# Performance work log

Measured on AMD Instinct MI355X. Metric: run time of the kernel, lower is better.

The kernel has to match this reference:

```python
import jax, jax.numpy as jnp
import numpy as np

N, E, B, H, L = 50000, 500000, 64, 64, 4


def setup_inputs() -> dict:
    key = jax.random.key(0)
    ks = jax.random.split(key, 32)
    def w(k, shp, fan_in):
        s = 1.0 / np.sqrt(fan_in)
        return jax.random.uniform(k, shp, jnp.float32, -s, s)
    inp = {
        "v0": jax.random.normal(ks[0], (N, 1), jnp.float32),
        "v1": jax.random.normal(ks[1], (N, 1), jnp.float32),
        "dist": jax.random.uniform(ks[2], (E, 1), jnp.float32),
        "edge_index": jax.random.randint(ks[3], (2, E), 0, N, jnp.int32),
        "batch": jnp.sort(jax.random.randint(ks[4], (N,), 0, B, jnp.int32)),
        "batch_size": B,
        # embeddings / per-input linears
        "wte": jax.random.normal(ks[5], (2, H), jnp.float32),
        "W_in0": w(ks[6], (H, 1), 1), "b_in0": w(ks[7], (H,), 1),
        "W_in1": w(ks[8], (H, 1), 1), "b_in1": w(ks[9], (H,), 1),
        "W_out0": w(ks[10], (1, H), H), "b_out0": w(ks[11], (1,), H),
        "W_out1": w(ks[12], (1, H), H), "b_out1": w(ks[13], (1,), H),
        "W_edge": w(ks[14], (H, 1), 1), "b_edge": w(ks[15], (H,), 1),
        # shared GraphBlock (ModuleList([block]*L) shares weights)
        "W_el": w(ks[16], (H, 2 * H), 2 * H), "b_el": w(ks[17], (H,), 2 * H),
        "W_n1": w(ks[18], (4 * H, 3 * H), 3 * H), "b_n1": w(ks[19], (4 * H,), 3 * H),
        "W_n2": w(ks[20], (H, 4 * H), 4 * H), "b_n2": w(ks[21], (H,), 4 * H),
        "W_gl": w(ks[22], (H, 2 * H), 2 * H), "b_gl": w(ks[23], (H,), 2 * H),
        # shared LSTMCell
        "W_ih": w(ks[24], (4 * H, H), H), "W_hh": w(ks[25], (4 * H, H), H),
        "b_ih": w(ks[26], (4 * H,), H), "b_hh": w(ks[27], (4 * H,), H),
    }
    return inp


def _forward(v0, v1, dist, edge_index, batch, batch_size,
             wte, W_in0, b_in0, W_in1, b_in1, W_out0, b_out0, W_out1, b_out1,
             W_edge, b_edge, W_el, b_el, W_n1, b_n1, W_n2, b_n2, W_gl, b_gl,
             W_ih, W_hh, b_ih, b_hh):
    # x = sum_i (type_embedding_i + Linear_i(v_i))  -> [N, H]
    x = (wte[0] + v0 @ W_in0.T + b_in0) + (wte[1] + v1 @ W_in1.T + b_in1)
    e = dist @ W_edge.T + b_edge                      # [E, H]
    u = jnp.zeros((batch_size, x.shape[-1]), x.dtype)  # [B, H]
    row, col = edge_index[0], edge_index[1]
    n_nodes = x.shape[0]
    cs = []
    for _ in range(L):  # shared weights across layers (faithful to [block]*L)
        # edge MLP on gathered source features, scatter-max to destination nodes
        msg = jax.nn.relu(jnp.concatenate([x[row], e], axis=-1) @ W_el.T + b_el)
        agg = jax.ops.segment_max(msg, col, num_segments=n_nodes)
        agg = jnp.where(jnp.isfinite(agg), agg, 0.0)  # empty segments -> 0
        # node MLP with residual
        h1 = jax.nn.relu(jnp.concatenate([agg, x, u[batch]], axis=-1) @ W_n1.T + b_n1)
        x = x + h1 @ W_n2.T + b_n2
        # global update: per-graph max over nodes
        x_u = jax.ops.segment_max(x, batch, num_segments=batch_size)
        x_u = jnp.where(jnp.isfinite(x_u), x_u, 0.0)
        u = u + jax.nn.relu(jnp.concatenate([x_u, u], axis=-1) @ W_gl.T + b_gl)
        # LSTMCell with zero initial (h, c) every layer (hidden_states=None path)
        gates = u @ W_ih.T + b_ih + b_hh  # h_prev = 0 so W_hh term vanishes
        i_g, f_g, g_g, o_g = jnp.split(gates, 4, axis=-1)
        c = jax.nn.sigmoid(i_g) * jnp.tanh(g_g)        # c_prev = 0
        u = jax.nn.sigmoid(o_g) * jnp.tanh(c)
        cs.append(c)
    outs = jnp.stack([x @ W_out0.T + b_out0, x @ W_out1.T + b_out1])  # [2, N, 1]
    return outs, jnp.stack(cs)  # ([2,N,1], [L,B,H])


def reference(v0, v1, dist, edge_index, batch, batch_size,
              wte, W_in0, b_in0, W_in1, b_in1, W_out0, b_out0, W_out1, b_out1,
              W_edge, b_edge, W_el, b_el, W_n1, b_n1, W_n2, b_n2, W_gl, b_gl,
              W_ih, W_hh, b_ih, b_hh):
    return _forward(v0, v1, dist, edge_index, batch, batch_size,
                    wte, W_in0, b_in0, W_in1, b_in1, W_out0, b_out0, W_out1, b_out1,
                    W_edge, b_edge, W_el, b_el, W_n1, b_n1, W_n2, b_n2, W_gl, b_gl,
                    W_ih, W_hh, b_ih, b_hh)
```

## Files before the change

kernel.cpp:

```cpp
#include <hip/hip_runtime.h>


typedef __attribute__((ext_vector_type(8))) short short8;
typedef __attribute__((ext_vector_type(4))) float f32x4;

__device__ __forceinline__ unsigned short f2bf(float f) {
  union { float f; unsigned u; } v; v.f = f;
  unsigned r = v.u + 0x7FFFu + ((v.u >> 16) & 1u);
  return (unsigned short)(r >> 16);
}
__device__ __forceinline__ float bf2f(unsigned short s) {
  return __uint_as_float((unsigned)s << 16);
}
__device__ __forceinline__ unsigned enc_ordered(float f) {
  unsigned u = __float_as_uint(f);
  return (u >> 31) ? ~u : (u | 0x80000000u);
}

__global__ void k_prep_pq(const float* __restrict__ W_el, const float* __restrict__ b_el,
                          const float* __restrict__ W_edge, const float* __restrict__ b_edge,
                          const float* __restrict__ wte,
                          const float* __restrict__ Wi0, const float* __restrict__ bi0,
                          const float* __restrict__ Wi1, const float* __restrict__ bi1,
                          float* __restrict__ p, float* __restrict__ q,
                          float* __restrict__ c0, float* __restrict__ c1,
                          float* __restrict__ c2) {
  int h = threadIdx.x;
  float pp = 0.f, qq = 0.f, s0 = 0.f, s1 = 0.f, s2 = 0.f;
  for (int k = 0; k < 64; ++k) {
    float w2 = W_el[h * 128 + 64 + k];
    pp += w2 * W_edge[k];
    qq += w2 * b_edge[k];
    float w1 = W_el[h * 128 + k];
    float base = wte[k] + wte[64 + k] + bi0[k] + bi1[k];
    s0 += w1 * base;
    s1 += w1 * Wi0[k];
    s2 += w1 * Wi1[k];
  }
  p[h] = pp; q[h] = qq + b_el[h];
  c0[h] = s0; c1[h] = s1; c2[h] = s2;
}

__global__ void k_init(const float* __restrict__ v0, const float* __restrict__ v1,
                       const float* __restrict__ wte,
                       const float* __restrict__ Wi0, const float* __restrict__ bi0,
                       const float* __restrict__ Wi1, const float* __restrict__ bi1,
                       const int* __restrict__ batch,
                       int* __restrict__ gstart, int* __restrict__ gend,
                       float* __restrict__ x,
                       float* __restrict__ u, unsigned* __restrict__ xu_enc,
                       unsigned short* __restrict__ W1b, unsigned short* __restrict__ W2b,
                       unsigned short* __restrict__ Welb,
                       const float* __restrict__ W_n1, const float* __restrict__ W_n2,
                       const float* __restrict__ W_el,
                       int* __restrict__ deg, int* __restrict__ cur, int N) {
  int gt = blockIdx.x * 256 + threadIdx.x;
  int NH = N * 64;
  if (gt < NH) {
    int n = gt >> 6, h = gt & 63;
    x[gt] = wte[h] + wte[64 + h] + bi0[h] + bi1[h] + v0[n] * Wi0[h] + v1[n] * Wi1[h];
    if (h == 0) {
      int bg = batch[n];
      if (n == 0 || batch[n - 1] != bg) gstart[bg] = n;
      if (n == N - 1 || batch[n + 1] != bg) gend[bg] = n + 1;
    }
    return;
  }
  int i = gt - NH;
  if (i < 4096) {
    u[i] = 0.f;
  } else if (i < 8192) {
    xu_enc[i - 4096] = 0x007FFFFFu;
  } else if (i < 8192 + 49152) {
    int j = i - 8192;
    W1b[j] = f2bf(W_n1[j]);
  } else if (i < 8192 + 49152 + 16384) {
    int j = i - 57344;
    W2b[j] = f2bf(W_n2[j]);
  } else if (i < 77824) {
    int j = i - 73728;
    Welb[j] = f2bf(W_el[(j >> 6) * 128 + (j & 63)]);
  } else if (i < 77824 + N) {
    deg[i - 77824] = 0;
  } else if (i < 77824 + 2 * N) {
    cur[i - 77824 - N] = 0;
  }
}

__global__ __launch_bounds__(256) void k_hist(const int* __restrict__ eidx,
                                              int* __restrict__ deg, int E) {
  int e = blockIdx.x * 256 + threadIdx.x;
  if (e < E) atomicAdd(&deg[eidx[E + e]], 1);
}

__global__ __launch_bounds__(256) void k_scan1(const int* __restrict__ deg,
                                               int* __restrict__ off,
                                               int* __restrict__ bsum, int N) {
  __shared__ int s[256];
  int b = blockIdx.x, t = threadIdx.x;
  int i0 = b * 512 + t * 2;
  int v0 = (i0 < N) ? deg[i0] : 0;
  int v1 = (i0 + 1 < N) ? deg[i0 + 1] : 0;
  int sum = v0 + v1;
  s[t] = sum;
  __syncthreads();
  for (int d = 1; d < 256; d <<= 1) {
    int val = (t >= d) ? s[t - d] : 0;
    __syncthreads();
    s[t] += val;
    __syncthreads();
  }
  int excl = s[t] - sum;
  if (i0 < N) off[i0] = excl + v0;
  if (i0 + 1 < N) off[i0 + 1] = excl + v0 + v1;
  if (t == 255) bsum[b] = s[t];
}

__global__ void k_scan2(int* __restrict__ bsum, int nb) {
  __shared__ int s[128];
  int t = threadIdx.x;
  int v = (t < nb) ? bsum[t] : 0;
  s[t] = v;
  __syncthreads();
  for (int d = 1; d < 128; d <<= 1) {
    int val = (t >= d) ? s[t - d] : 0;
    __syncthreads();
    s[t] += val;
    __syncthreads();
  }
  if (t < nb) bsum[t] = s[t] - v;
}

__global__ __launch_bounds__(256) void k_scatter(const int* __restrict__ eidx,
                                                 const float* __restrict__ dist,
                                                 const int* __restrict__ off,
                                                 const int* __restrict__ bsum,
                                                 int* __restrict__ cur,
                                                 uint2* __restrict__ spack, int E) {
  int e = blockIdx.x * 256 + threadIdx.x;
  if (e >= E) return;
  int c = eidx[E + e];
  int base = (c == 0) ? 0 : (off[c - 1] + bsum[(c - 1) >> 9]);
  int pos = base + atomicAdd(&cur[c], 1);
  spack[pos] = make_uint2((unsigned)eidx[e] | ((unsigned)(c & 31) << 27),
                          __float_as_uint(dist[e]));
}

#define PROC(cc, gg)                                                     \
  do {                                                                   \
    int _c = (int)(cc);                                                  \
    if (_c != ccur) {                                                    \
      if (ccur >= 0) atomicMax(&aggi[ccur * 64 + lane], __float_as_int(m)); \
      ccur = _c; m = (gg);                                               \
    } else m = fmaxf(m, (gg));                                           \
  } while (0)

template <int MODE>
__global__ __launch_bounds__(256) void k_node(
    const int* __restrict__ off, const int* __restrict__ bsum,
    const uint2* __restrict__ spack,
    const float* __restrict__ p, const float* __restrict__ q,
    const float* __restrict__ c0, const float* __restrict__ c1,
    const float* __restrict__ c2,
    const float* __restrict__ v0, const float* __restrict__ v1,
    float* __restrict__ x, unsigned short* __restrict__ y_bf,
    const int* __restrict__ batch, const float* __restrict__ u,
    const unsigned short* __restrict__ W1b, const unsigned short* __restrict__ W2b,
    const unsigned short* __restrict__ Welb,
    const float* __restrict__ b_n1, const float* __restrict__ b_n2,
    unsigned* __restrict__ xu_enc,
    float* __restrict__ bmaxA, float* __restrict__ bmaxB,
    int* __restrict__ bgidA, int* __restrict__ bgidB,
    const float* __restrict__ Wo0, const float* __restrict__ bo0,
    const float* __restrict__ Wo1, const float* __restrict__ bo1,
    float* __restrict__ outp, int N) {
  __shared__ __align__(16) char inb[32 * 384];
  __shared__ __align__(16) char h1T[32 * 512];
  __shared__ uint2 smeta[256];
  __shared__ int sgb[32];
  int t = threadIdx.x;
  int n0 = blockIdx.x * 32;
  int lane = t & 63, wv = t >> 6;
  int lr = lane & 15;
  int lk8 = (lane >> 4) << 3;
  int jo = (lane >> 4) << 2;
  int swzr = (lr & 7) << 4;
  int h0 = wv * 16 + jo;

  float4 xo[2];
#pragma unroll
  for (int nt = 0; nt < 2; ++nt) {
    int node = n0 + nt * 16 + lr;
    xo[nt] = (node < N) ? *(const float4*)(x + (size_t)node * 64 + h0)
                        : make_float4(0.f, 0.f, 0.f, 0.f);
  }
  int nd_s = t >> 3, ko = t & 7;
  int node_s = n0 + nd_s;
  float4 ua = make_float4(0.f, 0.f, 0.f, 0.f), ub = ua;
  if (node_s < N) {
    int g = batch[node_s];
    const float4* u4 = (const float4*)u;
    ua = u4[g * 16 + ko * 2];
    ub = u4[g * 16 + ko * 2 + 1];
  }
  if (t < 32) sgb[t] = batch[min(n0 + t, N - 1)];
  float pv = p[lane], qv = q[lane];
  float c0v = 0.f, c1v = 0.f, c2v = 0.f;
  if (MODE == 0) { c0v = c0[lane]; c1v = c1[lane]; c2v = c2[lane]; }

  int* aggi = (int*)h1T;
#pragma unroll
  for (int i = 0; i < 8; ++i) aggi[t + i * 256] = 0;

#pragma unroll
  for (int nt = 0; nt < 2; ++nt) {
    int nd = nt * 16 + lr;
    unsigned lo = (unsigned)f2bf(xo[nt].x) | ((unsigned)f2bf(xo[nt].y) << 16);
    unsigned hi = (unsigned)f2bf(xo[nt].z) | ((unsigned)f2bf(xo[nt].w) << 16);
    *(uint2*)(inb + nd * 384 + ((128 + h0 * 2) ^ ((nd & 7) << 4))) = make_uint2(lo, hi);
  }
  {
    int swz = (nd_s & 7) << 4;
    uint4 uv;
    uv.x = f2bf(ua.x) | ((unsigned)f2bf(ua.y) << 16);
    uv.y = f2bf(ua.z) | ((unsigned)f2bf(ua.w) << 16);
    uv.z = f2bf(ub.x) | ((unsigned)f2bf(ub.y) << 16);
    uv.w = f2bf(ub.z) | ((unsigned)f2bf(ub.w) << 16);
    *(uint4*)(inb + nd_s * 384 + ((256 + ko * 16) ^ swz)) = uv;
  }
  __syncthreads();

  {
    int last = min(n0 + 31, N - 1);
    int ebase = (n0 == 0) ? 0 : (off[n0 - 1] + bsum[(n0 - 1) >> 9]);
    int eend = off[last] + bsum[last >> 9];
    int total = eend - ebase;
    int q4 = total >> 2;
    int wb = ebase + wv * q4;
    int we = (wv == 3) ? eend : (wb + q4);
    uint2* sm = smeta + wv * 64;
    const unsigned short* ybl = y_bf + lane;
    float m = 0.f;
    int ccur = -1;
    uint2 r = make_uint2(0u, 0u);
    if (wb < we) {
      int cnt = min(64, we - wb);
      if (lane < cnt) r = spack[wb + lane];
    }
    for (int cb = wb; cb < we; cb += 64) {
      int ccnt = min(64, we - cb);
      sm[lane] = r;
      int nb = cb + 64;
      if (nb < we) {
        int ncnt = we - nb;
        if (lane < ncnt) r = spack[nb + lane];
      }
      int i = 0;
      for (; i + 8 <= ccnt; i += 8) {
        uint2 e0 = sm[i], e1 = sm[i + 1], e2 = sm[i + 2], e3 = sm[i + 3];
        uint2 e4 = sm[i + 4], e5 = sm[i + 5], e6 = sm[i + 6], e7 = sm[i + 7];
        float y0, y1, y2, y3, y4, y5, y6, y7;
        if (MODE == 0) {
          int r0 = e0.x & 0x07FFFFFFu, r1 = e1.x & 0x07FFFFFFu;
          int r2 = e2.x & 0x07FFFFFFu, r3 = e3.x & 0x07FFFFFFu;
          int r4 = e4.x & 0x07FFFFFFu, r5 = e5.x & 0x07FFFFFFu;
          int r6 = e6.x & 0x07FFFFFFu, r7 = e7.x & 0x07FFFFFFu;
          y0 = fmaf(v1[r0], c2v, fmaf(v0[r0], c1v, c0v));
          y1 = fmaf(v1[r1], c2v, fmaf(v0[r1], c1v, c0v));
          y2 = fmaf(v1[r2], c2v, fmaf(v0[r2], c1v, c0v));
          y3 = fmaf(v1[r3], c2v, fmaf(v0[r3], c1v, c0v));
          y4 = fmaf(v1[r4], c2v, fmaf(v0[r4], c1v, c0v));
          y5 = fmaf(v1[r5], c2v, fmaf(v0[r5], c1v, c0v));
          y6 = fmaf(v1[r6], c2v, fmaf(v0[r6], c1v, c0v));
          y7 = fmaf(v1[r7], c2v, fmaf(v0[r7], c1v, c0v));
        } else {
          y0 = bf2f(ybl[(int)((e0.x & 0x07FFFFFFu) << 6)]);
          y1 = bf2f(ybl[(int)((e1.x & 0x07FFFFFFu) << 6)]);
          y2 = bf2f(ybl[(int)((e2.x & 0x07FFFFFFu) << 6)]);
          y3 = bf2f(ybl[(int)((e3.x & 0x07FFFFFFu) << 6)]);
          y4 = bf2f(ybl[(int)((e4.x & 0x07FFFFFFu) << 6)]);
          y5 = bf2f(ybl[(int)((e5.x & 0x07FFFFFFu) << 6)]);
          y6 = bf2f(ybl[(int)((e6.x & 0x07FFFFFFu) << 6)]);
          y7 = bf2f(ybl[(int)((e7.x & 0x07FFFFFFu) << 6)]);
        }
        float g0 = fmaxf(fmaf(__uint_as_float(e0.y), pv, y0 + qv), 0.f);
        float g1 = fmaxf(fmaf(__uint_as_float(e1.y), pv, y1 + qv), 0.f);
        float g2 = fmaxf(fmaf(__uint_as_float(e2.y), pv, y2 + qv), 0.f);
        float g3 = fmaxf(fmaf(__uint_as_float(e3.y), pv, y3 + qv), 0.f);
        float g4 = fmaxf(fmaf(__uint_as_float(e4.y), pv, y4 + qv), 0.f);
        float g5 = fmaxf(fmaf(__uint_as_float(e5.y), pv, y5 + qv), 0.f);
        float g6 = fmaxf(fmaf(__uint_as_float(e6.y), pv, y6 + qv), 0.f);
        float g7 = fmaxf(fmaf(__uint_as_float(e7.y), pv, y7 + qv), 0.f);
        PROC(e0.x >> 27, g0); PROC(e1.x >> 27, g1);
        PROC(e2.x >> 27, g2); PROC(e3.x >> 27, g3);
        PROC(e4.x >> 27, g4); PROC(e5.x >> 27, g5);
        PROC(e6.x >> 27, g6); PROC(e7.x >> 27, g7);
      }
      for (; i < ccnt; ++i) {
        uint2 e0 = sm[i];
        float y0;
        if (MODE == 0) {
          int r0 = e0.x & 0x07FFFFFFu;
          y0 = fmaf(v1[r0], c2v, fmaf(v0[r0], c1v, c0v));
        } else {
          y0 = bf2f(ybl[(int)((e0.x & 0x07FFFFFFu) << 6)]);
        }
        float g0 = fmaxf(fmaf(__uint_as_float(e0.y), pv, y0 + qv), 0.f);
        PROC(e0.x >> 27, g0);
      }
    }
    if (ccur >= 0) atomicMax(&aggi[ccur * 64 + lane], __float_as_int(m));
  }
  __syncthreads();

  {
    int swz = (nd_s & 7) << 4;
    const float4* ag4 = (const float4*)(h1T);
    float4 aa = ag4[nd_s * 16 + ko * 2];
    float4 ab = ag4[nd_s * 16 + ko * 2 + 1];
    uint4 av;
    av.x = f2bf(aa.x) | ((unsigned)f2bf(aa.y) << 16);
    av.y = f2bf(aa.z) | ((unsigned)f2bf(aa.w) << 16);
    av.z = f2bf(ab.x) | ((unsigned)f2bf(ab.y) << 16);
    av.w = f2bf(ab.z) | ((unsigned)f2bf(ab.w) << 16);
    *(uint4*)(inb + nd_s * 384 + ((ko * 16) ^ swz)) = av;
  }
  __syncthreads();

  int w = wv;

  f32x4 acc[4][2];
#pragma unroll
  for (int ot = 0; ot < 4; ++ot)
#pragma unroll
    for (int nt = 0; nt < 2; ++nt) acc[ot][nt] = (f32x4){0.f, 0.f, 0.f, 0.f};
  const unsigned short* W1p = W1b + (w * 64 + lr) * 192 + lk8;
#pragma unroll
  for (int ks = 0; ks < 6; ++ks) {
    int kb = ks * 64 + lk8 * 2;
    short8 b0 = *(const short8*)(inb + lr * 384 + (kb ^ swzr));
    short8 b1 = *(const short8*)(inb + (16 + lr) * 384 + (kb ^ swzr));
#pragma unroll
    for (int ot = 0; ot < 4; ++ot) {
      short8 a = *(const short8*)(W1p + ot * (16 * 192) + ks * 32);
      acc[ot][0] = __builtin_amdgcn_mfma_f32_16x16x32_bf16(a, b0, acc[ot][0], 0, 0, 0);
      acc[ot][1] = __builtin_amdgcn_mfma_f32_16x16x32_bf16(a, b1, acc[ot][1], 0, 0, 0);
    }
  }
  __syncthreads();
#pragma unroll
  for (int ot = 0; ot < 4; ++ot) {
    int o = w * 64 + ot * 16 + jo;
    float4 bs = *(const float4*)(b_n1 + o);
#pragma unroll
    for (int nt = 0; nt < 2; ++nt) {
      int nd = nt * 16 + lr;
      unsigned lo = (unsigned)f2bf(fmaxf(acc[ot][nt][0] + bs.x, 0.f)) |
                    ((unsigned)f2bf(fmaxf(acc[ot][nt][1] + bs.y, 0.f)) << 16);
      unsigned hi = (unsigned)f2bf(fmaxf(acc[ot][nt][2] + bs.z, 0.f)) |
                    ((unsigned)f2bf(fmaxf(acc[ot][nt][3] + bs.w, 0.f)) << 16);
      *(uint2*)(h1T + nd * 512 + ((o * 2) ^ ((nd & 7) << 4))) = make_uint2(lo, hi);
    }
  }
  __syncthreads();

  f32x4 acc2[2] = {{0.f, 0.f, 0.f, 0.f}, {0.f, 0.f, 0.f, 0.f}};
  const unsigned short* W2p = W2b + (w * 16 + lr) * 256 + lk8;
#pragma unroll
  for (int ks = 0; ks < 8; ++ks) {
    short8 a = *(const short8*)(W2p + ks * 32);
    int kb = ks * 64 + lk8 * 2;
    short8 b0 = *(const short8*)(h1T + lr * 512 + (kb ^ swzr));
    short8 b1 = *(const short8*)(h1T + (16 + lr) * 512 + (kb ^ swzr));
    acc2[0] = __builtin_amdgcn_mfma_f32_16x16x32_bf16(a, b0, acc2[0], 0, 0, 0);
    acc2[1] = __builtin_amdgcn_mfma_f32_16x16x32_bf16(a, b1, acc2[1], 0, 0, 0);
  }
  float4 b2 = *(const float4*)(b_n2 + h0);
  char* xnb = inb;
  float4 xn[2];
#pragma unroll
  for (int nt = 0; nt < 2; ++nt) {
    int nd = nt * 16 + lr;
    int node = n0 + nd;
    xn[nt].x = xo[nt].x + acc2[nt][0] + b2.x;
    xn[nt].y = xo[nt].y + acc2[nt][1] + b2.y;
    xn[nt].z = xo[nt].z + acc2[nt][2] + b2.z;
    xn[nt].w = xo[nt].w + acc2[nt][3] + b2.w;
    if (node >= N) xn[nt] = make_float4(0.f, 0.f, 0.f, 0.f);
    if (MODE != 2 && node < N) *(float4*)(x + (size_t)node * 64 + h0) = xn[nt];
    if (MODE != 2) {
      unsigned lo = (unsigned)f2bf(xn[nt].x) | ((unsigned)f2bf(xn[nt].y) << 16);
      unsigned hi = (unsigned)f2bf(xn[nt].z) | ((unsigned)f2bf(xn[nt].w) << 16);
      *(uint2*)(xnb + nd * 128 + ((h0 * 2) ^ ((nd & 7) << 4))) = make_uint2(lo, hi);
    }
  }

  {
    const float NEG = -__builtin_huge_valf();
    int gA = sgb[0], gB = sgb[31];
    float a0 = NEG, a1 = NEG, a2 = NEG, a3 = NEG;
    float e0 = NEG, e1 = NEG, e2 = NEG, e3 = NEG;
#pragma unroll
    for (int nt = 0; nt < 2; ++nt) {
      int nd = nt * 16 + lr;
      if (n0 + nd < N) {
        int g = sgb[nd];
        if (g == gA) {
          a0 = fmaxf(a0, xn[nt].x); a1 = fmaxf(a1, xn[nt].y);
          a2 = fmaxf(a2, xn[nt].z); a3 = fmaxf(a3, xn[nt].w);
        } else if (g == gB) {
          e0 = fmaxf(e0, xn[nt].x); e1 = fmaxf(e1, xn[nt].y);
          e2 = fmaxf(e2, xn[nt].z); e3 = fmaxf(e3, xn[nt].w);
        } else {
          unsigned* xe = xu_enc + g * 64 + h0;
          atomicMax(xe + 0, enc_ordered(xn[nt].x));
          atomicMax(xe + 1, enc_ordered(xn[nt].y));
          atomicMax(xe + 2, enc_ordered(xn[nt].z));
          atomicMax(xe + 3, enc_ordered(xn[nt].w));
        }
      }
    }
#pragma unroll
    for (int msk = 1; msk <= 8; msk <<= 1) {
      a0 = fmaxf(a0, __shfl_xor(a0, msk)); a1 = fmaxf(a1, __shfl_xor(a1, msk));
      a2 = fmaxf(a2, __shfl_xor(a2, msk)); a3 = fmaxf(a3, __shfl_xor(a3, msk));
      e0 = fmaxf(e0, __shfl_xor(e0, msk)); e1 = fmaxf(e1, __shfl_xor(e1, msk));
      e2 = fmaxf(e2, __shfl_xor(e2, msk)); e3 = fmaxf(e3, __shfl_xor(e3, msk));
    }
    if (lr == 0) {
      size_t base = (size_t)blockIdx.x * 64 + h0;
      bmaxA[base + 0] = a0; bmaxA[base + 1] = a1;
      bmaxA[base + 2] = a2; bmaxA[base + 3] = a3;
      bmaxB[base + 0] = e0; bmaxB[base + 1] = e1;
      bmaxB[base + 2] = e2; bmaxB[base + 3] = e3;
    }
    if (t == 0) {
      bgidA[blockIdx.x] = gA;
      bgidB[blockIdx.x] = (gB == gA) ? -1 : gB;
    }
  }
  __syncthreads();

  if (MODE != 2) {
    f32x4 acc3[2] = {{0.f, 0.f, 0.f, 0.f}, {0.f, 0.f, 0.f, 0.f}};
    const unsigned short* W3p = Welb + (w * 16 + lr) * 64 + lk8;
#pragma unroll
    for (int ks = 0; ks < 2; ++ks) {
      short8 a = *(const short8*)(W3p + ks * 32);
      int kb = ks * 64 + lk8 * 2;
      short8 b0 = *(const short8*)(xnb + lr * 128 + (kb ^ swzr));
      short8 b1 = *(const short8*)(xnb + (16 + lr) * 128 + (kb ^ swzr));
      acc3[0] = __builtin_amdgcn_mfma_f32_16x16x32_bf16(a, b0, acc3[0], 0, 0, 0);
      acc3[1] = __builtin_amdgcn_mfma_f32_16x16x32_bf16(a, b1, acc3[1], 0, 0, 0);
    }
    int o0 = w * 16 + jo;
#pragma unroll
    for (int nt = 0; nt < 2; ++nt) {
      int node = n0 + nt * 16 + lr;
      if (node < N) {
        unsigned lo = (unsigned)f2bf(acc3[nt][0]) | ((unsigned)f2bf(acc3[nt][1]) << 16);
        unsigned hi = (unsigned)f2bf(acc3[nt][2]) | ((unsigned)f2bf(acc3[nt][3]) << 16);
        *(uint2*)(y_bf + (size_t)node * 64 + o0) = make_uint2(lo, hi);
      }
    }
  } else {
    float4 w0 = *(const float4*)(Wo0 + h0);
    float4 w1 = *(const float4*)(Wo1 + h0);
    float* ow = (float*)h1T;
#pragma unroll
    for (int nt = 0; nt < 2; ++nt) {
      float p0 = xn[nt].x * w0.x + xn[nt].y * w0.y + xn[nt].z * w0.z + xn[nt].w * w0.w;
      float p1 = xn[nt].x * w1.x + xn[nt].y * w1.y + xn[nt].z * w1.z + xn[nt].w * w1.w;
      p0 += __shfl_xor(p0, 16); p0 += __shfl_xor(p0, 32);
      p1 += __shfl_xor(p1, 16); p1 += __shfl_xor(p1, 32);
      if (lane < 16) {
        ow[w * 64 + 0 + nt * 16 + lr] = p0;
        ow[w * 64 + 32 + nt * 16 + lr] = p1;
      }
    }
    __syncthreads();
    if (t < 64) {
      int oi = t >> 5, nd = t & 31;
      int node = n0 + nd;
      if (node < N) {
        float v = ow[0 * 64 + oi * 32 + nd] + ow[1 * 64 + oi * 32 + nd] +
                  ow[2 * 64 + oi * 32 + nd] + ow[3 * 64 + oi * 32 + nd];
        v += (oi ? bo1[0] : bo0[0]);
        outp[(size_t)oi * N + node] = v;
      }
    }
  }
}

__global__ __launch_bounds__(256) void k_graph(const int* __restrict__ gstart,
                                               const int* __restrict__ gend,
                                               const float* __restrict__ bmaxA,
                                               const float* __restrict__ bmaxB,
                                               const int* __restrict__ bgidA,
                                               const int* __restrict__ bgidB,
                                               unsigned* __restrict__ xu_enc,
                                               float* __restrict__ u,
                                               const float* __restrict__ W_gl,
                                               const float* __restrict__ b_gl,
                                               const float* __restrict__ W_ih,
                                               const float* __restrict__ b_ih,
                                               const float* __restrict__ b_hh,
                                               float* __restrict__ c_out) {
  __shared__ float red[4][3][64];
  __shared__ float xu_s[64], us[64], un[64];
  int g = blockIdx.x;
  int t = threadIdx.x, h = t & 63, qd = t >> 6;
  const float NEG = -__builtin_huge_valf();

  float m = NEG;
  int gs = gstart[g], ge = gend[g];
  if (gs < ge) {
    int bs = gs >> 5, be = (ge - 1) >> 5;
    for (int b = bs + qd; b <= be; b += 4) {
      if (bgidA[b] == g) m = fmaxf(m, bmaxA[(size_t)b * 64 + h]);
      if (bgidB[b] == g) m = fmaxf(m, bmaxB[(size_t)b * 64 + h]);
    }
  }
  red[qd][0][h] = m;
  __syncthreads();
  if (qd == 0) {
    m = fmaxf(fmaxf(red[0][0][h], red[1][0][h]), fmaxf(red[2][0][h], red[3][0][h]));
    unsigned Ev = xu_enc[g * 64 + h];
    float fd = (Ev & 0x80000000u) ? __uint_as_float(Ev & 0x7FFFFFFFu)
                                  : __uint_as_float(~Ev);
    m = fmaxf(m, fd);
    xu_enc[g * 64 + h] = 0x007FFFFFu;
    xu_s[h] = isfinite(m) ? m : 0.f;
    us[h] = u[g * 64 + h];
  }
  __syncthreads();

  float pre = 0.f;
  {
    const float* Wrow = W_gl + h * 128 + qd * 32;
    const float* src = (qd < 2) ? (xu_s + qd * 32) : (us + (qd - 2) * 32);
#pragma unroll 8
    for (int k = 0; k < 32; ++k) pre += src[k] * Wrow[k];
  }
  red[qd][0][h] = pre;
  __syncthreads();
  if (qd == 0) {
    float prs = red[0][0][h] + red[1][0][h] + red[2][0][h] + red[3][0][h] + b_gl[h];
    un[h] = us[h] + fmaxf(prs, 0.f);
  }
  __syncthreads();

  float gi = 0.f, gg = 0.f, go = 0.f;
#pragma unroll 4
  for (int k = qd * 16; k < qd * 16 + 16; ++k) {
    float uv = un[k];
    gi += uv * W_ih[h * 64 + k];
    gg += uv * W_ih[(128 + h) * 64 + k];
    go += uv * W_ih[(192 + h) * 64 + k];
  }
  red[qd][0][h] = gi; red[qd][1][h] = gg; red[qd][2][h] = go;
  __syncthreads();
  if (qd == 0) {
    gi = red[0][0][h] + red[1][0][h] + red[2][0][h] + red[3][0][h] + b_ih[h] + b_hh[h];
    gg = red[0][1][h] + red[1][1][h] + red[2][1][h] + red[3][1][h] +
         b_ih[128 + h] + b_hh[128 + h];
    go = red[0][2][h] + red[1][2][h] + red[2][2][h] + red[3][2][h] +
         b_ih[192 + h] + b_hh[192 + h];
    float cc = (1.f / (1.f + expf(-gi))) * tanhf(gg);
    float u2v = (1.f / (1.f + expf(-go))) * tanhf(cc);
    c_out[g * 64 + h] = cc;
    u[g * 64 + h] = u2v;
  }
}

extern "C" void kernel_launch(void* const* d_in, const int* in_sizes, int n_in,
                              void* d_out, int out_size, void* d_ws, size_t ws_size,
                              hipStream_t stream) {
  const float* v0 = (const float*)d_in[0];
  const float* v1 = (const float*)d_in[1];
  const float* dist = (const float*)d_in[2];
  const int* eidx = (const int*)d_in[3];
  const int* batch = (const int*)d_in[4];
  const float* wte = (const float*)d_in[6];
  const float* Wi0 = (const float*)d_in[7];
  const float* bi0 = (const float*)d_in[8];
  const float* Wi1 = (const float*)d_in[9];
  const float* bi1 = (const float*)d_in[10];
  const float* Wo0 = (const float*)d_in[11];
  const float* bo0 = (const float*)d_in[12];
  const float* Wo1 = (const float*)d_in[13];
  const float* bo1 = (const float*)d_in[14];
  const float* W_edge = (const float*)d_in[15];
  const float* b_edge = (const float*)d_in[16];
  const float* W_el = (const float*)d_in[17];
  const float* b_el = (const float*)d_in[18];
  const float* W_n1 = (const float*)d_in[19];
  const float* b_n1 = (const float*)d_in[20];
  const float* W_n2 = (const float*)d_in[21];
  const float* b_n2 = (const float*)d_in[22];
  const float* W_gl = (const float*)d_in[23];
  const float* b_gl = (const float*)d_in[24];
  const float* W_ih = (const float*)d_in[25];
  const float* b_ih = (const float*)d_in[27];
  const float* b_hh = (const float*)d_in[28];

  const int N = in_sizes[0];
  const int E = in_sizes[2];
  const int NH = N * 64;
  const int NB512 = (N + 511) / 512;
  const int nblk = (N + 31) / 32;

  float* ws = (float*)d_ws;
  float* x = ws;
  float* u = x + NH;
  unsigned* xu_enc = (unsigned*)(u + 4096);
  float* p = (float*)(xu_enc + 4096);
  float* q = p + 64;
  float* c0 = q + 64;
  float* c1 = c0 + 64;
  float* c2 = c1 + 64;
  unsigned short* W1b = (unsigned short*)(c2 + 64);
  unsigned short* W2b = W1b + 49152;
  unsigned short* Welb = W2b + 16384;
  unsigned short* y_bf = Welb + 4096;
  int* deg = (int*)(y_bf + NH);
  int* off = deg + N;
  int* cur = off + N;
  int* bsum = cur + N;
  int* gstart = bsum + 128;
  int* gend = gstart + 64;
  int* bgidA = gend + 64;
  int* bgidB = bgidA + nblk;
  float* bmaxA = (float*)(bgidB + nblk);
  float* bmaxB = bmaxA + (size_t)nblk * 64;
  uint2* spack = (uint2*)(((size_t)(bmaxB + (size_t)nblk * 64) + 15) & ~(size_t)15);

  float* outp = (float*)d_out;

  k_prep_pq<<<1, 64, 0, stream>>>(W_el, b_el, W_edge, b_edge, wte, Wi0, bi0, Wi1, bi1,
                                  p, q, c0, c1, c2);
  k_init<<<(NH + 77824 + 2 * N + 255) / 256, 256, 0, stream>>>(
      v0, v1, wte, Wi0, bi0, Wi1, bi1, batch, gstart, gend, x,
      u, xu_enc, W1b, W2b, Welb, W_n1, W_n2, W_el, deg, cur, N);
  k_hist<<<(E + 255) / 256, 256, 0, stream>>>(eidx, deg, E);
  k_scan1<<<NB512, 256, 0, stream>>>(deg, off, bsum, N);
  k_scan2<<<1, 128, 0, stream>>>(bsum, NB512);
  k_scatter<<<(E + 255) / 256, 256, 0, stream>>>(eidx, dist, off, bsum, cur, spack, E);

  for (int l = 0; l < 4; ++l) {
    if (l == 0) {
      k_node<0><<<nblk, 256, 0, stream>>>(off, bsum, spack, p, q, c0, c1, c2, v0, v1,
                                          x, y_bf, batch, u, W1b, W2b, Welb, b_n1, b_n2,
                                          xu_enc, bmaxA, bmaxB, bgidA, bgidB,
                                          Wo0, bo0, Wo1, bo1, outp, N);
    } else if (l < 3) {
      k_node<1><<<nblk, 256, 0, stream>>>(off, bsum, spack, p, q, c0, c1, c2, v0, v1,
                                          x, y_bf, batch, u, W1b, W2b, Welb, b_n1, b_n2,
                                          xu_enc, bmaxA, bmaxB, bgidA, bgidB,
                                          Wo0, bo0, Wo1, bo1, outp, N);
    } else {
      k_node<2><<<nblk, 256, 0, stream>>>(off, bsum, spack, p, q, c0, c1, c2, v0, v1,
                                          x, y_bf, batch, u, W1b, W2b, Welb, b_n1, b_n2,
                                          xu_enc, bmaxA, bmaxB, bgidA, bgidB,
                                          Wo0, bo0, Wo1, bo1, outp, N);
    }
    k_graph<<<64, 256, 0, stream>>>(gstart, gend, bmaxA, bmaxB, bgidA, bgidB,
                                    xu_enc, u, W_gl, b_gl, W_ih, b_ih, b_hh,
                                    outp + 2 * N + l * 4096);
  }
}
```

Before: 337.5 us.

## Process two edges per wavefront with paired-channel loads; fold prep kernel into init

The edge max-aggregation loop now splits each 64-lane wavefront into two halves. Each half handles a different edge, and each lane covers two adjacent hidden channels, loading them with one 32-bit load of packed bf16 y values instead of a 16-bit load per channel. This halves the number of gather instructions per edge and doubles edge-level parallelism per wave, at the cost of two LDS atomics per segment flush and extra predication in the tail. The tiny single-block k_prep_pq kernel is merged into k_init as 64 extra threads, removing one launch.

```diff
diff --git a/kernel.cpp b/kernel.cpp
--- a/kernel.cpp
+++ b/kernel.cpp
@@ -15,30 +15,6 @@
 __device__ __forceinline__ unsigned enc_ordered(float f) {
   unsigned u = __float_as_uint(f);
   return (u >> 31) ? ~u : (u | 0x80000000u);
-}
-
-__global__ void k_prep_pq(const float* __restrict__ W_el, const float* __restrict__ b_el,
-                          const float* __restrict__ W_edge, const float* __restrict__ b_edge,
-                          const float* __restrict__ wte,
-                          const float* __restrict__ Wi0, const float* __restrict__ bi0,
-                          const float* __restrict__ Wi1, const float* __restrict__ bi1,
-                          float* __restrict__ p, float* __restrict__ q,
-                          float* __restrict__ c0, float* __restrict__ c1,
-                          float* __restrict__ c2) {
-  int h = threadIdx.x;
-  float pp = 0.f, qq = 0.f, s0 = 0.f, s1 = 0.f, s2 = 0.f;
-  for (int k = 0; k < 64; ++k) {
-    float w2 = W_el[h * 128 + 64 + k];
-    pp += w2 * W_edge[k];
-    qq += w2 * b_edge[k];
-    float w1 = W_el[h * 128 + k];
-    float base = wte[k] + wte[64 + k] + bi0[k] + bi1[k];
-    s0 += w1 * base;
-    s1 += w1 * Wi0[k];
-    s2 += w1 * Wi1[k];
-  }
-  p[h] = pp; q[h] = qq + b_el[h];
-  c0[h] = s0; c1[h] = s1; c2[h] = s2;
 }
 
 __global__ void k_init(const float* __restrict__ v0, const float* __restrict__ v1,
@@ -53,6 +29,11 @@
                        unsigned short* __restrict__ Welb,
                        const float* __restrict__ W_n1, const float* __restrict__ W_n2,
                        const float* __restrict__ W_el,
+                       const float* __restrict__ b_el,
+                       const float* __restrict__ W_edge, const float* __restrict__ b_edge,
+                       float* __restrict__ p, float* __restrict__ q,
+                       float* __restrict__ c0, float* __restrict__ c1,
+                       float* __restrict__ c2,
                        int* __restrict__ deg, int* __restrict__ cur, int N) {
   int gt = blockIdx.x * 256 + threadIdx.x;
   int NH = N * 64;
@@ -84,6 +65,21 @@
     deg[i - 77824] = 0;
   } else if (i < 77824 + 2 * N) {
     cur[i - 77824 - N] = 0;
+  } else if (i < 77824 + 2 * N + 64) {
+    int h = i - 77824 - 2 * N;
+    float pp = 0.f, qq = 0.f, s0 = 0.f, s1 = 0.f, s2 = 0.f;
+    for (int k = 0; k < 64; ++k) {
+      float w2 = W_el[h * 128 + 64 + k];
+      pp += w2 * W_edge[k];
+      qq += w2 * b_edge[k];
+      float w1 = W_el[h * 128 + k];
+      float base = wte[k] + wte[64 + k] + bi0[k] + bi1[k];
+      s0 += w1 * base;
+      s1 += w1 * Wi0[k];
+      s2 += w1 * Wi1[k];
+    }
+    p[h] = pp; q[h] = qq + b_el[h];
+    c0[h] = s0; c1[h] = s1; c2[h] = s2;
   }
 }
 
@@ -145,15 +141,6 @@
   spack[pos] = make_uint2((unsigned)eidx[e] | ((unsigned)(c & 31) << 27),
                           __float_as_uint(dist[e]));
 }
-
-#define PROC(cc, gg)                                                     \
-  do {                                                                   \
-    int _c = (int)(cc);                                                  \
-    if (_c != ccur) {                                                    \
-      if (ccur >= 0) atomicMax(&aggi[ccur * 64 + lane], __float_as_int(m)); \
-      ccur = _c; m = (gg);                                               \
-    } else m = fmaxf(m, (gg));                                           \
-  } while (0)
 
 template <int MODE>
 __global__ __launch_bounds__(256) void k_node(
@@ -204,9 +191,6 @@
     ub = u4[g * 16 + ko * 2 + 1];
   }
   if (t < 32) sgb[t] = batch[min(n0 + t, N - 1)];
-  float pv = p[lane], qv = q[lane];
-  float c0v = 0.f, c1v = 0.f, c2v = 0.f;
-  if (MODE == 0) { c0v = c0[lane]; c1v = c1[lane]; c2v = c2[lane]; }
 
   int* aggi = (int*)h1T;
 #pragma unroll
@@ -239,8 +223,17 @@
     int wb = ebase + wv * q4;
     int we = (wv == 3) ? eend : (wb + q4);
     uint2* sm = smeta + wv * 64;
-    const unsigned short* ybl = y_bf + lane;
-    float m = 0.f;
+    int half = lane >> 5, l31 = lane & 31;
+    const unsigned* y32 = (const unsigned*)y_bf + l31;
+    float2 p2 = *(const float2*)(p + 2 * l31);
+    float2 q2 = *(const float2*)(q + 2 * l31);
+    float2 c02 = make_float2(0.f, 0.f), c12 = c02, c22 = c02;
+    if (MODE == 0) {
+      c02 = *(const float2*)(c0 + 2 * l31);
+      c12 = *(const float2*)(c1 + 2 * l31);
+      c22 = *(const float2*)(c2 + 2 * l31);
+    }
+    float m0 = 0.f, m1 = 0.f;
     int ccur = -1;
     uint2 r = make_uint2(0u, 0u);
     if (wb < we) {
@@ -255,61 +248,73 @@
         int ncnt = we - nb;
         if (lane < ncnt) r = spack[nb + lane];
       }
+      int nfull = ccnt >> 1;
       int i = 0;
-      for (; i + 8 <= ccnt; i += 8) {
-        uint2 e0 = sm[i], e1 = sm[i + 1], e2 = sm[i + 2], e3 = sm[i + 3];
-        uint2 e4 = sm[i + 4], e5 = sm[i + 5], e6 = sm[i + 6], e7 = sm[i + 7];
-        float y0, y1, y2, y3, y4, y5, y6, y7;
+      for (; i + 8 <= nfull; i += 8) {
+        uint2 e[8]; unsigned yd[8]; float va[8], vb[8];
+#pragma unroll
+        for (int k = 0; k < 8; ++k) e[k] = sm[2 * (i + k) + half];
+#pragma unroll
+        for (int k = 0; k < 8; ++k) {
+          unsigned row = e[k].x & 0x07FFFFFFu;
+          if (MODE == 0) { va[k] = v0[row]; vb[k] = v1[row]; }
+          else yd[k] = y32[row << 5];
+        }
+#pragma unroll
+        for (int k = 0; k < 8; ++k) {
+          float y0f, y1f;
+          if (MODE == 0) {
+            y0f = fmaf(vb[k], c22.x, fmaf(va[k], c12.x, c02.x));
+            y1f = fmaf(vb[k], c22.y, fmaf(va[k], c12.y, c02.y));
+          } else {
+            y0f = __uint_as_float(yd[k] << 16);
+            y1f = __uint_as_float(yd[k] & 0xFFFF0000u);
+          }
+          float d = __uint_as_float(e[k].y);
+          float g0 = fmaxf(fmaf(d, p2.x, y0f + q2.x), 0.f);
+          float g1 = fmaxf(fmaf(d, p2.y, y1f + q2.y), 0.f);
+          int c = (int)(e[k].x >> 27);
+          if (c != ccur) {
+            if (ccur >= 0) {
+              atomicMax(&aggi[ccur * 64 + 2 * l31], __float_as_int(m0));
+              atomicMax(&aggi[ccur * 64 + 2 * l31 + 1], __float_as_int(m1));
+            }
+            ccur = c; m0 = g0; m1 = g1;
+          } else { m0 = fmaxf(m0, g0); m1 = fmaxf(m1, g1); }
+        }
+      }
+      for (; 2 * i < ccnt; ++i) {
+        int idx = 2 * i + half;
+        bool val = idx < ccnt;
+        uint2 e = sm[val ? idx : 0];
+        unsigned row = e.x & 0x07FFFFFFu;
+        float y0f, y1f;
         if (MODE == 0) {
-          int r0 = e0.x & 0x07FFFFFFu, r1 = e1.x & 0x07FFFFFFu;
-          int r2 = e2.x & 0x07FFFFFFu, r3 = e3.x & 0x07FFFFFFu;
-          int r4 = e4.x & 0x07FFFFFFu, r5 = e5.x & 0x07FFFFFFu;
-          int r6 = e6.x & 0x07FFFFFFu, r7 = e7.x & 0x07FFFFFFu;
-          y0 = fmaf(v1[r0], c2v, fmaf(v0[r0], c1v, c0v));
-          y1 = fmaf(v1[r1], c2v, fmaf(v0[r1], c1v, c0v));
-          y2 = fmaf(v1[r2], c2v, fmaf(v0[r2], c1v, c0v));
-          y3 = fmaf(v1[r3], c2v, fmaf(v0[r3], c1v, c0v));
-          y4 = fmaf(v1[r4], c2v, fmaf(v0[r4], c1v, c0v));
-          y5 = fmaf(v1[r5], c2v, fmaf(v0[r5], c1v, c0v));
-          y6 = fmaf(v1[r6], c2v, fmaf(v0[r6], c1v, c0v));
-          y7 = fmaf(v1[r7], c2v, fmaf(v0[r7], c1v, c0v));
+          float a = v0[row], b = v1[row];
+          y0f = fmaf(b, c22.x, fmaf(a, c12.x, c02.x));
+          y1f = fmaf(b, c22.y, fmaf(a, c12.y, c02.y));
         } else {
-          y0 = bf2f(ybl[(int)((e0.x & 0x07FFFFFFu) << 6)]);
-          y1 = bf2f(ybl[(int)((e1.x & 0x07FFFFFFu) << 6)]);
-          y2 = bf2f(ybl[(int)((e2.x & 0x07FFFFFFu) << 6)]);
-          y3 = bf2f(ybl[(int)((e3.x & 0x07FFFFFFu) << 6)]);
-          y4 = bf2f(ybl[(int)((e4.x & 0x07FFFFFFu) << 6)]);
-          y5 = bf2f(ybl[(int)((e5.x & 0x07FFFFFFu) << 6)]);
-          y6 = bf2f(ybl[(int)((e6.x & 0x07FFFFFFu) << 6)]);
-          y7 = bf2f(ybl[(int)((e7.x & 0x07FFFFFFu) << 6)]);
+          unsigned yd = y32[row << 5];
+          y0f = __uint_as_float(yd << 16);
+          y1f = __uint_as_float(yd & 0xFFFF0000u);
         }
-        float g0 = fmaxf(fmaf(__uint_as_float(e0.y), pv, y0 + qv), 0.f);
-        float g1 = fmaxf(fmaf(__uint_as_float(e1.y), pv, y1 + qv), 0.f);
-        float g2 = fmaxf(fmaf(__uint_as_float(e2.y), pv, y2 + qv), 0.f);
-        float g3 = fmaxf(fmaf(__uint_as_float(e3.y), pv, y3 + qv), 0.f);
-        float g4 = fmaxf(fmaf(__uint_as_float(e4.y), pv, y4 + qv), 0.f);
-        float g5 = fmaxf(fmaf(__uint_as_float(e5.y), pv, y5 + qv), 0.f);
-        float g6 = fmaxf(fmaf(__uint_as_float(e6.y), pv, y6 + qv), 0.f);
-        float g7 = fmaxf(fmaf(__uint_as_float(e7.y), pv, y7 + qv), 0.f);
-        PROC(e0.x >> 27, g0); PROC(e1.x >> 27, g1);
-        PROC(e2.x >> 27, g2); PROC(e3.x >> 27, g3);
-        PROC(e4.x >> 27, g4); PROC(e5.x >> 27, g5);
-        PROC(e6.x >> 27, g6); PROC(e7.x >> 27, g7);
+        float d = __uint_as_float(e.y);
+        float g0 = val ? fmaxf(fmaf(d, p2.x, y0f + q2.x), 0.f) : 0.f;
+        float g1 = val ? fmaxf(fmaf(d, p2.y, y1f + q2.y), 0.f) : 0.f;
+        int c = val ? (int)(e.x >> 27) : ccur;
+        if (c != ccur) {
+          if (ccur >= 0) {
+            atomicMax(&aggi[ccur * 64 + 2 * l31], __float_as_int(m0));
+            atomicMax(&aggi[ccur * 64 + 2 * l31 + 1], __float_as_int(m1));
+          }
+          ccur = c; m0 = g0; m1 = g1;
+        } else { m0 = fmaxf(m0, g0); m1 = fmaxf(m1, g1); }
       }
-      for (; i < ccnt; ++i) {
-        uint2 e0 = sm[i];
-        float y0;
-        if (MODE == 0) {
-          int r0 = e0.x & 0x07FFFFFFu;
-          y0 = fmaf(v1[r0], c2v, fmaf(v0[r0], c1v, c0v));
-        } else {
-          y0 = bf2f(ybl[(int)((e0.x & 0x07FFFFFFu) << 6)]);
-        }
-        float g0 = fmaxf(fmaf(__uint_as_float(e0.y), pv, y0 + qv), 0.f);
-        PROC(e0.x >> 27, g0);
-      }
-    }
-    if (ccur >= 0) atomicMax(&aggi[ccur * 64 + lane], __float_as_int(m));
+    }
+    if (ccur >= 0) {
+      atomicMax(&aggi[ccur * 64 + 2 * l31], __float_as_int(m0));
+      atomicMax(&aggi[ccur * 64 + 2 * l31 + 1], __float_as_int(m1));
+    }
   }
   __syncthreads();
 
@@ -637,11 +642,10 @@
 
   float* outp = (float*)d_out;
 
-  k_prep_pq<<<1, 64, 0, stream>>>(W_el, b_el, W_edge, b_edge, wte, Wi0, bi0, Wi1, bi1,
-                                  p, q, c0, c1, c2);
-  k_init<<<(NH + 77824 + 2 * N + 255) / 256, 256, 0, stream>>>(
+  k_init<<<(NH + 77824 + 2 * N + 64 + 255) / 256, 256, 0, stream>>>(
       v0, v1, wte, Wi0, bi0, Wi1, bi1, batch, gstart, gend, x,
-      u, xu_enc, W1b, W2b, Welb, W_n1, W_n2, W_el, deg, cur, N);
+      u, xu_enc, W1b, W2b, Welb, W_n1, W_n2, W_el, b_el, W_edge, b_edge,
+      p, q, c0, c1, c2, deg, cur, N);
   k_hist<<<(E + 255) / 256, 256, 0, stream>>>(eidx, deg, E);
   k_scan1<<<NB512, 256, 0, stream>>>(deg, off, bsum, N);
   k_scan2<<<1, 128, 0, stream>>>(bsum, NB512);
```

Measured after the change: 313.9 us. 7.0% less time.
